# Kernel optimization log

Hardware: AMD Instinct MI355X
Metric: run time of the kernel (lower is better)

The kernel has to match this reference:

```python
import jax, jax.numpy as jnp
import numpy as np

B, HN, N1, N2, S = 32, 12, 256, 320, 256  # S = hardcoded 256 buffer size
EPS = 1e-5


def setup_inputs() -> dict:
    key = jax.random.key(0)
    ks = jax.random.split(key, 6)
    attn_rgb = jax.random.normal(ks[0], (B, HN, N1, N2), dtype=jnp.float32)
    attn_tir = jax.random.normal(ks[1], (B, HN, N1, N2), dtype=jnp.float32)
    # per-batch unique indices in [0, 256): permutation (collision-free scatter)
    perm = jax.vmap(lambda k: jax.random.permutation(k, S))(jax.random.split(ks[2], B))
    global_index_s = perm[:, :N1].astype(jnp.int32)
    # LayerNorm(512) params
    ln_g = jnp.ones((2 * S,), jnp.float32)
    ln_b = jnp.zeros((2 * S,), jnp.float32)
    # Linear(512,256) xavier-uniform weight, zero bias (stored as [in,out])
    lim1 = float(np.sqrt(6.0 / (2 * S + S)))
    W1 = jax.random.uniform(ks[3], (2 * S, S), jnp.float32, -lim1, lim1)
    b1 = jnp.zeros((S,), jnp.float32)
    # Linear(256,512)
    lim2 = float(np.sqrt(6.0 / (S + 2 * S)))
    W2 = jax.random.uniform(ks[4], (S, 2 * S), jnp.float32, -lim2, lim2)
    b2 = jnp.zeros((2 * S,), jnp.float32)
    return {"attn_rgb": attn_rgb, "attn_tir": attn_tir, "global_index_s": global_index_s,
            "ln_g": ln_g, "ln_b": ln_b, "W1": W1, "b1": b1, "W2": W2, "b2": b2}


def reference(attn_rgb, attn_tir, global_index_s, ln_g, ln_b, W1, b1, W2, b2):
    Bv, hn, n1, _ = attn_rgb.shape
    idx = jnp.broadcast_to(global_index_s[:, None, :].astype(jnp.int32), (Bv, hn, n1))  # [B,hn,N1]
    # detach() in torch source -> stop_gradient on the max-pooled path
    mx_rgb = jax.lax.stop_gradient(attn_rgb).max(-1)  # [B,hn,N1]
    mx_tir = jax.lax.stop_gradient(attn_tir).max(-1)
    bi = jnp.arange(Bv)[:, None, None]
    hi = jnp.arange(hn)[None, :, None]
    vex_rgb = jnp.zeros((Bv, hn, S), attn_rgb.dtype).at[bi, hi, idx].set(mx_rgb)
    vex_tir = jnp.zeros((Bv, hn, S), attn_tir.dtype).at[bi, hi, idx].set(mx_tir)
    v = jnp.concatenate([vex_rgb, vex_tir], axis=-1)  # [B,hn,512]
    # LayerNorm(512)
    mu = v.mean(-1, keepdims=True)
    var = v.var(-1, keepdims=True)
    v = (v - mu) * jax.lax.rsqrt(var + EPS) * ln_g + ln_b
    # SE MLP: Linear -> ReLU -> Linear -> Sigmoid
    h = jax.nn.relu(jnp.einsum('bhe,ef->bhf', v, W1) + b1)
    g = jax.nn.sigmoid(jnp.einsum('bhf,fe->bhe', h, W2) + b2)  # [B,hn,512]
    # gather gates back via indices and modulate
    g_rgb = jnp.take_along_axis(g[..., :S], idx, axis=-1)[..., None]  # [B,hn,N1,1]
    g_tir = jnp.take_along_axis(g[..., S:], idx, axis=-1)[..., None]
    attn_rgb_col = g_rgb * attn_rgb
    attn_tir_col = g_tir * attn_tir
    return (attn_tir_col, attn_rgb_col)
```

## Files before the change

### kernel.cpp

```cpp
#include <hip/hip_runtime.h>
#include <hip/hip_bf16.h>
#include <math.h>

#define BB   32
#define HN   12
#define N1   256
#define N2   320
#define SS   256
#define BH   (BB*HN)
#define ROWS (BH*N1)
#define N4PT ((BH*N1*N2)/4)

typedef float v4f __attribute__((ext_vector_type(4)));

__global__ __launch_bounds__(256) void k_rowmax(
    const float* __restrict__ rgb, const float* __restrict__ tir,
    float* __restrict__ mxr, float* __restrict__ mxt)
{
    int wid  = (blockIdx.x * 256 + threadIdx.x) >> 6;
    int lane = threadIdx.x & 63;
    int isTir = wid >= ROWS;
    int row  = isTir ? wid - ROWS : wid;
    const v4f* p = (const v4f*)((isTir ? tir : rgb) + (size_t)row * N2);
    v4f a = p[lane];
    float m = fmaxf(fmaxf(a.x, a.y), fmaxf(a.z, a.w));
    if (lane < 16) {
        v4f b = p[64 + lane];
        m = fmaxf(m, fmaxf(fmaxf(b.x, b.y), fmaxf(b.z, b.w)));
    }
#pragma unroll
    for (int off = 32; off; off >>= 1) m = fmaxf(m, __shfl_xor(m, off));
    if (lane == 0) (isTir ? mxt : mxr)[row] = m;
}

__global__ __launch_bounds__(256) void k_mlp(
    const int*   __restrict__ gidx,
    const float* __restrict__ mxr, const float* __restrict__ mxt,
    const float* __restrict__ ln_g, const float* __restrict__ ln_b,
    const float* __restrict__ W1,  const float* __restrict__ b1,
    const float* __restrict__ W2,  const float* __restrict__ b2,
    float* __restrict__ grgb, float* __restrict__ gtir)
{
    __shared__ float v[4][2 * SS];
    __shared__ float hs[4][SS];
    __shared__ float gs[4][2 * SS];

    const int t   = threadIdx.x;
    const int bh0 = blockIdx.x * 4;

#pragma unroll
    for (int r = 0; r < 4; ++r) { v[r][t] = 0.f; v[r][t + SS] = 0.f; }
    __syncthreads();
#pragma unroll
    for (int r = 0; r < 4; ++r) {
        int bh   = bh0 + r;
        int b    = bh / HN;
        int sidx = gidx[b * SS + t];
        v[r][sidx]      = mxr[bh * N1 + t];
        v[r][sidx + SS] = mxt[bh * N1 + t];
    }
    __syncthreads();

    {
        int w = t >> 6, l = t & 63;
        float xs[8];
        float s = 0.f, sq = 0.f;
#pragma unroll
        for (int k = 0; k < 8; ++k) {
            xs[k] = v[w][l + 64 * k];
            s += xs[k]; sq = fmaf(xs[k], xs[k], sq);
        }
#pragma unroll
        for (int off = 32; off; off >>= 1) {
            s  += __shfl_xor(s, off);
            sq += __shfl_xor(sq, off);
        }
        float mu   = s * (1.f / 512.f);
        float var  = sq * (1.f / 512.f) - mu * mu;
        float rstd = rsqrtf(var + 1e-5f);
#pragma unroll
        for (int k = 0; k < 8; ++k) {
            int i = l + 64 * k;
            v[w][i] = (xs[k] - mu) * rstd * ln_g[i] + ln_b[i];
        }
    }
    __syncthreads();

    {
        float acc0 = b1[t], acc1 = acc0, acc2 = acc0, acc3 = acc0;
#pragma unroll 4
        for (int e4 = 0; e4 < 128; ++e4) {
            v4f v0 = *(const v4f*)&v[0][e4 * 4];
            v4f v1 = *(const v4f*)&v[1][e4 * 4];
            v4f v2 = *(const v4f*)&v[2][e4 * 4];
            v4f v3 = *(const v4f*)&v[3][e4 * 4];
            float w0 = W1[(e4 * 4 + 0) * SS + t];
            float w1 = W1[(e4 * 4 + 1) * SS + t];
            float w2 = W1[(e4 * 4 + 2) * SS + t];
            float w3 = W1[(e4 * 4 + 3) * SS + t];
            acc0 = fmaf(v0.x, w0, acc0); acc0 = fmaf(v0.y, w1, acc0);
            acc0 = fmaf(v0.z, w2, acc0); acc0 = fmaf(v0.w, w3, acc0);
            acc1 = fmaf(v1.x, w0, acc1); acc1 = fmaf(v1.y, w1, acc1);
            acc1 = fmaf(v1.z, w2, acc1); acc1 = fmaf(v1.w, w3, acc1);
            acc2 = fmaf(v2.x, w0, acc2); acc2 = fmaf(v2.y, w1, acc2);
            acc2 = fmaf(v2.z, w2, acc2); acc2 = fmaf(v2.w, w3, acc2);
            acc3 = fmaf(v3.x, w0, acc3); acc3 = fmaf(v3.y, w1, acc3);
            acc3 = fmaf(v3.z, w2, acc3); acc3 = fmaf(v3.w, w3, acc3);
        }
        hs[0][t] = fmaxf(acc0, 0.f);
        hs[1][t] = fmaxf(acc1, 0.f);
        hs[2][t] = fmaxf(acc2, 0.f);
        hs[3][t] = fmaxf(acc3, 0.f);
    }
    __syncthreads();

    {
        float alo0 = b2[t],      alo1 = alo0, alo2 = alo0, alo3 = alo0;
        float ahi0 = b2[t + SS], ahi1 = ahi0, ahi2 = ahi0, ahi3 = ahi0;
#pragma unroll 4
        for (int f4 = 0; f4 < 64; ++f4) {
            v4f h0 = *(const v4f*)&hs[0][f4 * 4];
            v4f h1 = *(const v4f*)&hs[1][f4 * 4];
            v4f h2 = *(const v4f*)&hs[2][f4 * 4];
            v4f h3 = *(const v4f*)&hs[3][f4 * 4];
#pragma unroll
            for (int q = 0; q < 4; ++q) {
                int f = f4 * 4 + q;
                float wlo = W2[f * 2 * SS + t];
                float whi = W2[f * 2 * SS + t + SS];
                float e0 = (q == 0) ? h0.x : (q == 1) ? h0.y : (q == 2) ? h0.z : h0.w;
                float e1 = (q == 0) ? h1.x : (q == 1) ? h1.y : (q == 2) ? h1.z : h1.w;
                float e2 = (q == 0) ? h2.x : (q == 1) ? h2.y : (q == 2) ? h2.z : h2.w;
                float e3 = (q == 0) ? h3.x : (q == 1) ? h3.y : (q == 2) ? h3.z : h3.w;
                alo0 = fmaf(e0, wlo, alo0); ahi0 = fmaf(e0, whi, ahi0);
                alo1 = fmaf(e1, wlo, alo1); ahi1 = fmaf(e1, whi, ahi1);
                alo2 = fmaf(e2, wlo, alo2); ahi2 = fmaf(e2, whi, ahi2);
                alo3 = fmaf(e3, wlo, alo3); ahi3 = fmaf(e3, whi, ahi3);
            }
        }
        gs[0][t] = 1.f / (1.f + expf(-alo0)); gs[0][t + SS] = 1.f / (1.f + expf(-ahi0));
        gs[1][t] = 1.f / (1.f + expf(-alo1)); gs[1][t + SS] = 1.f / (1.f + expf(-ahi1));
        gs[2][t] = 1.f / (1.f + expf(-alo2)); gs[2][t + SS] = 1.f / (1.f + expf(-ahi2));
        gs[3][t] = 1.f / (1.f + expf(-alo3)); gs[3][t + SS] = 1.f / (1.f + expf(-ahi3));
    }
    __syncthreads();

#pragma unroll
    for (int r = 0; r < 4; ++r) {
        int bh   = bh0 + r;
        int b    = bh / HN;
        int sidx = gidx[b * SS + t];
        grgb[bh * N1 + t] = gs[r][sidx];
        gtir[bh * N1 + t] = gs[r][sidx + SS];
    }
}

__global__ __launch_bounds__(256) void k_mod(
    const float* __restrict__ rgb, const float* __restrict__ tir,
    const float* __restrict__ grgb, const float* __restrict__ gtir,
    v4f* __restrict__ out)
{
    int i = blockIdx.x * 256 + threadIdx.x;
    int isRgb = i >= N4PT;
    int j = isRgb ? i - N4PT : i;
    int row = j / 80;
    const v4f* src = (const v4f*)(isRgb ? rgb : tir);
    float gate = isRgb ? grgb[row] : gtir[row];
    v4f a = src[j];
    v4f o = a * gate;
    __builtin_nontemporal_store(o, &out[i]);
}

extern "C" void kernel_launch(void* const* d_in, const int* in_sizes, int n_in,
                              void* d_out, int out_size, void* d_ws, size_t ws_size,
                              hipStream_t stream)
{
    const float* attn_rgb = (const float*)d_in[0];
    const float* attn_tir = (const float*)d_in[1];
    const int*   gidx     = (const int*)  d_in[2];
    const float* ln_g     = (const float*)d_in[3];
    const float* ln_b     = (const float*)d_in[4];
    const float* W1       = (const float*)d_in[5];
    const float* b1       = (const float*)d_in[6];
    const float* W2       = (const float*)d_in[7];
    const float* b2       = (const float*)d_in[8];

    float* ws   = (float*)d_ws;
    float* mxr  = ws;
    float* mxt  = mxr + ROWS;
    float* grgb = mxt + ROWS;
    float* gtir = grgb + ROWS;

    int k1_blocks = (2 * ROWS) / 4;
    k_rowmax<<<k1_blocks, 256, 0, stream>>>(attn_rgb, attn_tir, mxr, mxt);

    k_mlp<<<BH / 4, 256, 0, stream>>>(gidx, mxr, mxt, ln_g, ln_b, W1, b1, W2, b2,
                                      grgb, gtir);

    int k3_blocks = (2 * N4PT) / 256;
    k_mod<<<k3_blocks, 256, 0, stream>>>(attn_rgb, attn_tir, grgb, gtir,
                                         (v4f*)d_out);
}
```

Before: 161.4 us.

## Stage inputs into output during rowmax, then scale output in place

The row-max pass now also copies both input tensors into the output buffer, using nontemporal loads. The final modulation pass becomes an in-place scale of the output, so it no longer rereads the original inputs. This aims to keep the second pass's data resident in cache, but it adds an extra full write and read of the output and raises total DRAM traffic if that data is not cached.

```diff
diff --git a/kernel.cpp b/kernel.cpp
--- a/kernel.cpp
+++ b/kernel.cpp
@@ -9,23 +9,29 @@
 #define SS   256
 #define BH   (BB*HN)
 #define ROWS (BH*N1)
-#define N4PT ((BH*N1*N2)/4)
+#define R4   (N2/4)
+#define N4PT ((size_t)ROWS*R4)
 
 typedef float v4f __attribute__((ext_vector_type(4)));
 
-__global__ __launch_bounds__(256) void k_rowmax(
+__global__ __launch_bounds__(256) void k_stage(
     const float* __restrict__ rgb, const float* __restrict__ tir,
-    float* __restrict__ mxr, float* __restrict__ mxt)
-{
-    int wid  = (blockIdx.x * 256 + threadIdx.x) >> 6;
+    float* __restrict__ mxr, float* __restrict__ mxt,
+    v4f* __restrict__ outTir, v4f* __restrict__ outRgb)
+{
+    int wid  = ((int)blockIdx.x * 256 + (int)threadIdx.x) >> 6;
     int lane = threadIdx.x & 63;
     int isTir = wid >= ROWS;
     int row  = isTir ? wid - ROWS : wid;
-    const v4f* p = (const v4f*)((isTir ? tir : rgb) + (size_t)row * N2);
-    v4f a = p[lane];
+    const v4f* p  = (const v4f*)((isTir ? tir : rgb) + (size_t)row * N2);
+    v4f*       st = (isTir ? outTir : outRgb) + (size_t)row * R4;
+
+    v4f a = __builtin_nontemporal_load(&p[lane]);
+    st[lane] = a;
     float m = fmaxf(fmaxf(a.x, a.y), fmaxf(a.z, a.w));
     if (lane < 16) {
-        v4f b = p[64 + lane];
+        v4f b = __builtin_nontemporal_load(&p[64 + lane]);
+        st[64 + lane] = b;
         m = fmaxf(m, fmaxf(fmaxf(b.x, b.y), fmaxf(b.z, b.w)));
     }
 #pragma unroll
@@ -155,20 +161,23 @@
     }
 }
 
-__global__ __launch_bounds__(256) void k_mod(
-    const float* __restrict__ rgb, const float* __restrict__ tir,
+__global__ __launch_bounds__(256) void k_scale(
     const float* __restrict__ grgb, const float* __restrict__ gtir,
-    v4f* __restrict__ out)
-{
-    int i = blockIdx.x * 256 + threadIdx.x;
-    int isRgb = i >= N4PT;
-    int j = isRgb ? i - N4PT : i;
-    int row = j / 80;
-    const v4f* src = (const v4f*)(isRgb ? rgb : tir);
-    float gate = isRgb ? grgb[row] : gtir[row];
-    v4f a = src[j];
-    v4f o = a * gate;
-    __builtin_nontemporal_store(o, &out[i]);
+    v4f* __restrict__ outTir, v4f* __restrict__ outRgb)
+{
+    int wid  = ((int)blockIdx.x * 256 + (int)threadIdx.x) >> 6;
+    int lane = threadIdx.x & 63;
+    int isTir = wid >= ROWS;
+    int row  = isTir ? wid - ROWS : wid;
+    v4f*  o = (isTir ? outTir : outRgb) + (size_t)row * R4;
+    float g = (isTir ? gtir : grgb)[row];
+
+    v4f a = o[lane];
+    o[lane] = a * g;
+    if (lane < 16) {
+        v4f b = o[64 + lane];
+        o[64 + lane] = b * g;
+    }
 }
 
 extern "C" void kernel_launch(void* const* d_in, const int* in_sizes, int n_in,
@@ -191,13 +200,15 @@
     float* grgb = mxt + ROWS;
     float* gtir = grgb + ROWS;
 
+    v4f* outTir = (v4f*)d_out;
+    v4f* outRgb = outTir + N4PT;
+
     int k1_blocks = (2 * ROWS) / 4;
-    k_rowmax<<<k1_blocks, 256, 0, stream>>>(attn_rgb, attn_tir, mxr, mxt);
+    k_stage<<<k1_blocks, 256, 0, stream>>>(attn_rgb, attn_tir, mxr, mxt,
+                                           outTir, outRgb);
 
     k_mlp<<<BH / 4, 256, 0, stream>>>(gidx, mxr, mxt, ln_g, ln_b, W1, b1, W2, b2,
                                       grgb, gtir);
 
-    int k3_blocks = (2 * N4PT) / 256;
-    k_mod<<<k3_blocks, 256, 0, stream>>>(attn_rgb, attn_tir, grgb, gtir,
-                                         (v4f*)d_out);
-}
+    k_scale<<<k1_blocks, 256, 0, stream>>>(grgb, gtir, outTir, outRgb);
+}
```

Result: slower. 183.9 us (+14.0%).
